# Optimization experiments

Hardware: AMD Instinct MI355X
Metric: run time of the kernel (lower is better)

Reference implementation:

```python
import jax, jax.numpy as jnp
import numpy as np

D_MODEL = 1024
N_HEADS = 16
D_HEAD = D_MODEL // N_HEADS
D_FF = 4096
BATCH = 2
SEQ = 2048
LN_EPS = 1e-5


def setup_inputs() -> dict:
    key = jax.random.key(0)
    ks = jax.random.split(key, 12)
    s = 1.0 / np.sqrt(D_MODEL)
    x = jax.random.normal(ks[0], (BATCH, SEQ, D_MODEL), dtype=jnp.float32)
    mask = jnp.broadcast_to(jnp.tril(jnp.ones((SEQ, SEQ), jnp.int32)), (BATCH, SEQ, SEQ))
    return {
        "x": x,
        "mask": mask,
        # per-head projections stacked: [H, D, Dh] (bias=False in source)
        "Wq": jax.random.normal(ks[1], (N_HEADS, D_MODEL, D_HEAD), jnp.float32) * s,
        "Wk": jax.random.normal(ks[2], (N_HEADS, D_MODEL, D_HEAD), jnp.float32) * s,
        "Wv": jax.random.normal(ks[3], (N_HEADS, D_MODEL, D_HEAD), jnp.float32) * s,
        "Wo": jax.random.normal(ks[4], (D_MODEL, D_MODEL), jnp.float32) * s,
        "ln1_w": jnp.ones((D_MODEL,), jnp.float32),
        "ln1_b": jnp.zeros((D_MODEL,), jnp.float32),
        "ln2_w": jnp.ones((D_MODEL,), jnp.float32),
        "ln2_b": jnp.zeros((D_MODEL,), jnp.float32),
        "W1": jax.random.normal(ks[5], (D_MODEL, D_FF), jnp.float32) * s,
        "b1": jnp.zeros((D_FF,), jnp.float32),
        "W2": jax.random.normal(ks[6], (D_FF, D_MODEL), jnp.float32) * (1.0 / np.sqrt(D_FF)),
        "b2": jnp.zeros((D_MODEL,), jnp.float32),
    }


def layer_norm(x, w, b):
    mu = jnp.mean(x, axis=-1, keepdims=True)
    var = jnp.var(x, axis=-1, keepdims=True)
    return (x - mu) * jax.lax.rsqrt(var + LN_EPS) * w + b


def reference(x, mask, Wq, Wk, Wv, Wo, ln1_w, ln1_b, ln2_w, ln2_b, W1, b1, W2, b2):
    # pre-LN masked self-attention
    h = layer_norm(x, ln1_w, ln1_b)
    q = jnp.einsum("bsd,hde->bhse", h, Wq)  # [B,H,S,Dh]
    k = jnp.einsum("bsd,hde->bhse", h, Wk)
    v = jnp.einsum("bsd,hde->bhse", h, Wv)
    scores = jnp.einsum("bhse,bhte->bhst", q, k) / np.sqrt(D_HEAD)
    scores = jnp.where(mask[:, None, :, :].astype(bool), scores, -jnp.inf)
    weights = jax.nn.softmax(scores, axis=-1)
    attn = jnp.einsum("bhst,bhte->bhse", weights, v)  # [B,H,S,Dh]
    # concat heads (head order = last-dim order in torch.cat)
    concat = attn.transpose(0, 2, 1, 3).reshape(x.shape[0], x.shape[1], D_MODEL)
    att_out = concat @ Wo
    att_x = x + att_out
    # FFN with exact (erf) GELU, matching nn.GELU default
    h2 = layer_norm(att_x, ln2_w, ln2_b)
    ff = jax.nn.gelu(h2 @ W1 + b1, approximate=False) @ W2 + b2
    return att_x + ff
```

## Files before the change

kernel.cpp:

```cpp
#include <hip/hip_runtime.h>
#include <hip/hip_bf16.h>
#include <math.h>

#define D_MODEL 1024
#define N_HEADS 16
#define D_HEAD  64
#define D_FF    4096
#define BATCH   2
#define SEQ     2048
#define NTOK    (BATCH*SEQ)

typedef __hip_bfloat16 bf16;
typedef __attribute__((ext_vector_type(8))) short short8;
typedef __attribute__((ext_vector_type(4))) float floatx4;

template<typename TIN>
__global__ void ln_kernel(const TIN* __restrict__ x,
                          const float* __restrict__ w,
                          const float* __restrict__ b,
                          bf16* __restrict__ out) {
    int row = blockIdx.x;
    int tid = threadIdx.x;
    const long base = (long)row * D_MODEL;
    float v[4];
    float s = 0.f, sq = 0.f;
#pragma unroll
    for (int i = 0; i < 4; ++i) {
        float xv = (float)x[base + tid + i*256];
        v[i] = xv; s += xv; sq += xv*xv;
    }
    __shared__ float r1[256], r2[256];
    r1[tid] = s; r2[tid] = sq; __syncthreads();
    for (int off = 128; off > 0; off >>= 1) {
        if (tid < off) { r1[tid] += r1[tid+off]; r2[tid] += r2[tid+off]; }
        __syncthreads();
    }
    float mean = r1[0] * (1.f/D_MODEL);
    float var  = r2[0] * (1.f/D_MODEL) - mean*mean;
    float rstd = rsqrtf(var + 1e-5f);
#pragma unroll
    for (int i = 0; i < 4; ++i) {
        int c = tid + i*256;
        out[base + c] = __float2bfloat16((v[i] - mean) * rstd * w[c] + b[c]);
    }
}

__global__ __launch_bounds__(256) void wcvt_kernel(const float* __restrict__ W,
                                                   bf16* __restrict__ Wt,
                                                   int K, int N) {
    __shared__ float t[32][33];
    int n0 = blockIdx.x * 32, k0 = blockIdx.y * 32;
    int lx = threadIdx.x & 31, ly = threadIdx.x >> 5;
#pragma unroll
    for (int i = 0; i < 4; ++i) {
        int k = ly + i * 8;
        t[k][lx] = W[(long)(k0 + k) * N + n0 + lx];
    }
    __syncthreads();
#pragma unroll
    for (int i = 0; i < 4; ++i) {
        int n = ly + i * 8;
        Wt[(long)(n0 + n) * K + k0 + lx] = __float2bfloat16(t[lx][n]);
    }
}

__global__ __launch_bounds__(256) void wcvt_wo_w1(const float* __restrict__ Wo,
                                                  const float* __restrict__ W1,
                                                  bf16* __restrict__ wo_bf,
                                                  bf16* __restrict__ w1_bf) {
    __shared__ float t[32][33];
    int gx = blockIdx.x;
    const float* W; bf16* Wt; int N, n0;
    if (gx < 32) { W = Wo; Wt = wo_bf; N = D_MODEL; n0 = gx * 32; }
    else         { W = W1; Wt = w1_bf; N = D_FF;    n0 = (gx - 32) * 32; }
    int k0 = blockIdx.y * 32;
    int lx = threadIdx.x & 31, ly = threadIdx.x >> 5;
#pragma unroll
    for (int i = 0; i < 4; ++i) {
        int k = ly + i * 8;
        t[k][lx] = W[(long)(k0 + k) * N + n0 + lx];
    }
    __syncthreads();
#pragma unroll
    for (int i = 0; i < 4; ++i) {
        int n = ly + i * 8;
        Wt[(long)(n0 + n) * D_MODEL + k0 + lx] = __float2bfloat16(t[lx][n]);
    }
}

__global__ __launch_bounds__(256) void wcvt_qkv(const float* __restrict__ Wq,
                                                const float* __restrict__ Wk,
                                                const float* __restrict__ Wv,
                                                bf16* __restrict__ outp) {
    __shared__ float t[32][33];
    int z = blockIdx.z, mat = z >> 4, head = z & 15;
    const float* W = (mat == 0 ? Wq : mat == 1 ? Wk : Wv) + (long)head * D_MODEL * D_HEAD;
    bf16* Wt = outp + (long)z * D_HEAD * D_MODEL;
    int n0 = blockIdx.x * 32, k0 = blockIdx.y * 32;
    int lx = threadIdx.x & 31, ly = threadIdx.x >> 5;
#pragma unroll
    for (int i = 0; i < 4; ++i) {
        int k = ly + i * 8;
        t[k][lx] = W[(long)(k0 + k) * D_HEAD + n0 + lx];
    }
    __syncthreads();
#pragma unroll
    for (int i = 0; i < 4; ++i) {
        int n = ly + i * 8;
        Wt[(long)(n0 + n) * D_MODEL + k0 + lx] = __float2bfloat16(t[lx][n]);
    }
}

template<int ROWS>
__device__ inline void stage_tile(const bf16* g, int gstride, short* lds) {
    int lane = threadIdx.x & 63, wave = threadIdx.x >> 6;
#pragma unroll
    for (int it = 0; it < ROWS / 64; ++it) {
        int c = wave + it * 4;
        const bf16* gp = g + (long)(c * 16 + (lane >> 2)) * gstride + (lane & 3) * 8;
        short* lp = lds + c * 512 + lane * 8;
        __builtin_amdgcn_global_load_lds(
            (const __attribute__((address_space(1))) void*)gp,
            (__attribute__((address_space(3))) void*)lp, 16, 0, 0);
    }
}

template<int BM, int BN>
__device__ inline void gemm_accum(const bf16* __restrict__ A, int lda,
                                  const bf16* __restrict__ Wt, int K,
                                  int row0, int col0, short* As, short* Bs,
                                  floatx4 (&acc)[BM/32][BN/32]) {
    constexpr int MI = BM / 32;
    constexpr int NR = BN / 32;
    int tid  = threadIdx.x;
    int wave = tid >> 6, lane = tid & 63;
    int quad = lane >> 4, l16 = lane & 15;
    int wm = (wave >> 1) * (BM / 2);
    int wn = (wave & 1) * (BN / 2);

    for (int k0 = 0; k0 < K; k0 += 64) {
        stage_tile<BM>(A  + (long)row0 * lda + k0,      lda, As);
        stage_tile<BM>(A  + (long)row0 * lda + k0 + 32, lda, As + BM * 32);
        stage_tile<BN>(Wt + (long)col0 * K   + k0,      K,   Bs);
        stage_tile<BN>(Wt + (long)col0 * K   + k0 + 32, K,   Bs + BN * 32);
        __syncthreads();

#pragma unroll
        for (int p = 0; p < 2; ++p) {
            const short* Ap = As + p * BM * 32;
            const short* Bp = Bs + p * BN * 32;
            short8 af[MI], bfr[NR];
#pragma unroll
            for (int mi = 0; mi < MI; ++mi)
                af[mi] = *(const short8*)&Ap[(wm + mi * 16 + l16) * 32 + quad * 8];
#pragma unroll
            for (int ni = 0; ni < NR; ++ni)
                bfr[ni] = *(const short8*)&Bp[(wn + ni * 16 + l16) * 32 + quad * 8];
#pragma unroll
            for (int mi = 0; mi < MI; ++mi)
#pragma unroll
                for (int ni = 0; ni < NR; ++ni)
                    acc[mi][ni] = __builtin_amdgcn_mfma_f32_16x16x32_bf16(
                        af[mi], bfr[ni], acc[mi][ni], 0, 0, 0);
        }
        __syncthreads();
    }
}

template<int BM, int BN, int BIAS, int ACT, int RES, int OUTBF16>
__global__ __launch_bounds__(256) void mfma_gemm_bf(
    const bf16* __restrict__ A, int lda,
    const bf16* __restrict__ Wt, int K,
    const float* __restrict__ bias, const float* __restrict__ resid,
    void* __restrict__ Cout, int ldc)
{
    constexpr int MI = BM / 32;
    constexpr int NR = BN / 32;
    __shared__ short As[BM * 64];
    __shared__ short Bs[BN * 64];
    int row0 = blockIdx.y * BM, col0 = blockIdx.x * BN;
    int tid = threadIdx.x, wave = tid >> 6, lane = tid & 63;
    int quad = lane >> 4, l16 = lane & 15;
    int wm = (wave >> 1) * (BM / 2);
    int wn = (wave & 1) * (BN / 2);

    floatx4 acc[MI][NR];
#pragma unroll
    for (int mi = 0; mi < MI; ++mi)
#pragma unroll
        for (int ni = 0; ni < NR; ++ni)
            acc[mi][ni] = (floatx4){0.f, 0.f, 0.f, 0.f};

    gemm_accum<BM, BN>(A, lda, Wt, K, row0, col0, As, Bs, acc);

#pragma unroll
    for (int mi = 0; mi < MI; ++mi) {
#pragma unroll
        for (int ni = 0; ni < NR; ++ni) {
#pragma unroll
            for (int r = 0; r < 4; ++r) {
                int row = row0 + wm + mi * 16 + quad * 4 + r;
                int col = col0 + wn + ni * 16 + l16;
                float v = acc[mi][ni][r];
                if (BIAS) v += bias[col];
                if (ACT == 1) {
                    float x2 = v * v;
                    float arg = fminf(v * fmaf(0.1029392f, x2, 2.3021182f), 20.f);
                    float t = exp2f(arg);
                    v = v * t * __builtin_amdgcn_rcpf(t + 1.f);
                }
                long idx = (long)row * ldc + col;
                if (RES == 1) v += resid[idx];
                if (OUTBF16) ((bf16*)Cout)[idx] = __float2bfloat16(v);
                else         ((float*)Cout)[idx] = v;
            }
        }
    }
}

struct QkvOut { bf16* o[3]; };
__global__ __launch_bounds__(256) void qkv_kernel(const bf16* __restrict__ h1,
                                                  const bf16* __restrict__ wqkv,
                                                  QkvOut a) {
    __shared__ short As[128 * 64];
    __shared__ short Bs[128 * 64];
    int row0 = blockIdx.y * 128, col0 = blockIdx.x * 128;
    int tid = threadIdx.x, wave = tid >> 6, lane = tid & 63;
    int quad = lane >> 4, l16 = lane & 15;
    int wm = (wave >> 1) * 64, wn = (wave & 1) * 64;

    floatx4 acc[4][4];
#pragma unroll
    for (int mi = 0; mi < 4; ++mi)
#pragma unroll
        for (int ni = 0; ni < 4; ++ni)
            acc[mi][ni] = (floatx4){0.f, 0.f, 0.f, 0.f};

    gemm_accum<128, 128>(h1, D_MODEL, wqkv, D_MODEL, row0, col0, As, Bs, acc);

#pragma unroll
    for (int mi = 0; mi < 4; ++mi) {
#pragma unroll
        for (int ni = 0; ni < 4; ++ni) {
#pragma unroll
            for (int r = 0; r < 4; ++r) {
                int row = row0 + wm + mi * 16 + quad * 4 + r;
                int c   = col0 + wn + ni * 16 + l16;
                int mat = c >> 10, hd = (c >> 6) & 15, d = c & 63;
                int b = row >> 11, s = row & 2047;
                a.o[mat][(((long)(b * 16 + hd) * SEQ + s) << 6) + d] =
                    __float2bfloat16(acc[mi][ni][r]);
            }
        }
    }
}

__global__ __launch_bounds__(256) void fattn_mfma(const bf16* __restrict__ q,
                                                  const bf16* __restrict__ k,
                                                  const bf16* __restrict__ v,
                                                  bf16* __restrict__ concat) {
    int byr = blockIdx.y;
    int tile = (byr < 8) ? byr : 23 - byr;
    int bh = blockIdx.x;
    int b  = bh >> 4, h = bh & 15;
    int tid = threadIdx.x;
    int wave = tid >> 6, lane = tid & 63;
    int quad = lane >> 4, l16 = lane & 15;
    const long base = (long)bh * SEQ * D_HEAD;
    const int r0g = tile * 128;

    __shared__ short Ks[64 * 72];
    __shared__ short Vt[64 * 72];
    __shared__ short Ps[4][32 * 72];

    short8 qf[2][2];
#pragma unroll
    for (int rb = 0; rb < 2; ++rb) {
        const short* qrow = (const short*)(q + base +
            (long)(r0g + wave * 32 + rb * 16 + l16) * D_HEAD);
        qf[rb][0] = *(const short8*)(qrow + quad * 8);
        qf[rb][1] = *(const short8*)(qrow + 32 + quad * 8);
#pragma unroll
        for (int c = 0; c < 2; ++c)
#pragma unroll
            for (int j = 0; j < 8; ++j) {
                float f = __uint_as_float(((unsigned)(unsigned short)qf[rb][c][j]) << 16)
                          * 0.18033688f;
                qf[rb][c][j] = __builtin_bit_cast(short, __float2bfloat16(f));
            }
    }

    short8 onesf;
    {
        short o1 = (l16 == 0) ? (short)0x3F80 : (short)0;
#pragma unroll
        for (int j = 0; j < 8; ++j) onesf[j] = o1;
    }

    floatx4 o[2][4];
#pragma unroll
    for (int rb = 0; rb < 2; ++rb)
#pragma unroll
        for (int nb = 0; nb < 4; ++nb) o[rb][nb] = (floatx4){0.f, 0.f, 0.f, 0.f};
    floatx4 l4[2] = {(floatx4){0.f,0.f,0.f,0.f}, (floatx4){0.f,0.f,0.f,0.f}};

    const int ktmax = 2 * tile + 1;
    for (int kt = 0; kt <= ktmax; ++kt) {
        __syncthreads();
        {
            int t = tid >> 2, c = tid & 3;
            const short* krow = (const short*)(k + base + (long)(kt * 64 + t) * D_HEAD);
            *(uint4*)&Ks[t * 72 + c * 16]     = *(const uint4*)(krow + c * 16);
            *(uint4*)&Ks[t * 72 + c * 16 + 8] = *(const uint4*)(krow + c * 16 + 8);
        }
        {
            int tp = (tid & 31) * 2;
            int d0 = ((tid >> 5) & 7) * 8;
            const short* v0 = (const short*)(v + base + (long)(kt * 64 + tp) * D_HEAD + d0);
            short va[8], vb[8];
            *(uint4*)va = *(const uint4*)v0;
            *(uint4*)vb = *(const uint4*)(v0 + D_HEAD);
#pragma unroll
            for (int j = 0; j < 8; ++j) {
                unsigned pk = (unsigned)(unsigned short)va[j] |
                              ((unsigned)(unsigned short)vb[j] << 16);
                *(unsigned*)&Vt[(d0 + j) * 72 + tp] = pk;
            }
        }
        __syncthreads();

        if (kt * 64 > r0g + wave * 32 + 31) continue;

        floatx4 s[2][4];
#pragma unroll
        for (int nb = 0; nb < 4; ++nb) {
            short8 kf0 = *(const short8*)&Ks[(nb * 16 + l16) * 72 + quad * 8];
            short8 kf1 = *(const short8*)&Ks[(nb * 16 + l16) * 72 + 32 + quad * 8];
#pragma unroll
            for (int rb = 0; rb < 2; ++rb) {
                floatx4 z4 = (floatx4){0.f, 0.f, 0.f, 0.f};
                z4 = __builtin_amdgcn_mfma_f32_16x16x32_bf16(qf[rb][0], kf0, z4, 0, 0, 0);
                z4 = __builtin_amdgcn_mfma_f32_16x16x32_bf16(qf[rb][1], kf1, z4, 0, 0, 0);
                s[rb][nb] = z4;
            }
        }

        if (kt >= 2 * tile) {
#pragma unroll
            for (int rb = 0; rb < 2; ++rb) {
                int qg = r0g + wave * 32 + rb * 16 + quad * 4;
#pragma unroll
                for (int nb = 0; nb < 4; ++nb) {
                    int kg = kt * 64 + nb * 16 + l16;
#pragma unroll
                    for (int r = 0; r < 4; ++r)
                        if (kg > qg + r) s[rb][nb][r] = -1e30f;
                }
            }
        }

        short* Pw = &Ps[wave][0];
#pragma unroll
        for (int rb = 0; rb < 2; ++rb)
#pragma unroll
            for (int nb = 0; nb < 4; ++nb)
#pragma unroll
                for (int r = 0; r < 4; ++r) {
                    float p = exp2f(s[rb][nb][r]);
                    Pw[(rb * 16 + quad * 4 + r) * 72 + nb * 16 + l16] =
                        __builtin_bit_cast(short, __float2bfloat16(p));
                }

        short8 pf[2][2];
#pragma unroll
        for (int rb = 0; rb < 2; ++rb) {
            pf[rb][0] = *(const short8*)&Pw[(rb * 16 + l16) * 72 + quad * 8];
            pf[rb][1] = *(const short8*)&Pw[(rb * 16 + l16) * 72 + 32 + quad * 8];
        }
#pragma unroll
        for (int nb = 0; nb < 4; ++nb) {
            short8 vf0 = *(const short8*)&Vt[(nb * 16 + l16) * 72 + quad * 8];
            short8 vf1 = *(const short8*)&Vt[(nb * 16 + l16) * 72 + 32 + quad * 8];
#pragma unroll
            for (int rb = 0; rb < 2; ++rb) {
                o[rb][nb] = __builtin_amdgcn_mfma_f32_16x16x32_bf16(pf[rb][0], vf0, o[rb][nb], 0, 0, 0);
                o[rb][nb] = __builtin_amdgcn_mfma_f32_16x16x32_bf16(pf[rb][1], vf1, o[rb][nb], 0, 0, 0);
            }
        }
#pragma unroll
        for (int rb = 0; rb < 2; ++rb) {
            l4[rb] = __builtin_amdgcn_mfma_f32_16x16x32_bf16(pf[rb][0], onesf, l4[rb], 0, 0, 0);
            l4[rb] = __builtin_amdgcn_mfma_f32_16x16x32_bf16(pf[rb][1], onesf, l4[rb], 0, 0, 0);
        }
    }

#pragma unroll
    for (int rb = 0; rb < 2; ++rb) {
        float linv[4];
#pragma unroll
        for (int r = 0; r < 4; ++r) {
            float lv = __shfl(l4[rb][r], lane & 48);
            linv[r] = 1.f / lv;
        }
#pragma unroll
        for (int nb = 0; nb < 4; ++nb)
#pragma unroll
            for (int r = 0; r < 4; ++r) {
                int row = r0g + wave * 32 + rb * 16 + quad * 4 + r;
                int col = h * D_HEAD + nb * 16 + l16;
                concat[(long)(b * SEQ + row) * D_MODEL + col] =
                    __float2bfloat16(o[rb][nb][r] * linv[r]);
            }
    }
}

extern "C" void kernel_launch(void* const* d_in, const int* in_sizes, int n_in,
                              void* d_out, int out_size, void* d_ws, size_t ws_size,
                              hipStream_t stream) {
    const float* x    = (const float*)d_in[0];
    const float* Wq   = (const float*)d_in[2];
    const float* Wk   = (const float*)d_in[3];
    const float* Wv   = (const float*)d_in[4];
    const float* Wo   = (const float*)d_in[5];
    const float* ln1w = (const float*)d_in[6];
    const float* ln1b = (const float*)d_in[7];
    const float* ln2w = (const float*)d_in[8];
    const float* ln2b = (const float*)d_in[9];
    const float* W1   = (const float*)d_in[10];
    const float* b1   = (const float*)d_in[11];
    const float* W2   = (const float*)d_in[12];
    const float* b2   = (const float*)d_in[13];
    float* out = (float*)d_out;

    char* wsb = (char*)d_ws;
    const size_t MB = 1024*1024;
    bf16*  h1      = (bf16*)(wsb + 0*MB);
    bf16*  qb      = (bf16*)(wsb + 8*MB);
    bf16*  kb      = (bf16*)(wsb + 16*MB);
    bf16*  vb      = (bf16*)(wsb + 24*MB);
    bf16*  wqkv_bf = (bf16*)(wsb + 32*MB);
    bf16*  cc      = (bf16*)(wsb + 0*MB);
    bf16*  wo_bf   = (bf16*)(wsb + 8*MB);
    bf16*  w1_bf   = (bf16*)(wsb + 10*MB);
    bf16*  h2      = (bf16*)(wsb + 0*MB);
    bf16*  ff      = (bf16*)(wsb + 24*MB);
    bf16*  w2_bf   = (bf16*)(wsb + 8*MB);

    ln_kernel<float><<<NTOK, 256, 0, stream>>>(x, ln1w, ln1b, h1);

    wcvt_qkv<<<dim3(2, 32, 48), 256, 0, stream>>>(Wq, Wk, Wv, wqkv_bf);

    QkvOut qa; qa.o[0] = qb; qa.o[1] = kb; qa.o[2] = vb;
    qkv_kernel<<<dim3(24, 32), 256, 0, stream>>>(h1, wqkv_bf, qa);

    fattn_mfma<<<dim3(BATCH*N_HEADS, SEQ/128), 256, 0, stream>>>(qb, kb, vb, cc);

    wcvt_wo_w1<<<dim3(160, 32), 256, 0, stream>>>(Wo, W1, wo_bf, w1_bf);

    mfma_gemm_bf<64,128,0,0,1,0><<<dim3(8,64), 256, 0, stream>>>(
        cc, D_MODEL, wo_bf, D_MODEL, nullptr, x, out, D_MODEL);

    ln_kernel<float><<<NTOK, 256, 0, stream>>>(out, ln2w, ln2b, h2);

    mfma_gemm_bf<128,128,1,1,0,1><<<dim3(32,32), 256, 0, stream>>>(
        h2, D_MODEL, w1_bf, D_MODEL, b1, nullptr, ff, D_FF);

    wcvt_kernel<<<dim3(D_MODEL/32, D_FF/32), 256, 0, stream>>>(W2, w2_bf, D_FF, D_MODEL);

    mfma_gemm_bf<64,128,1,0,1,0><<<dim3(8,64), 256, 0, stream>>>(
        ff, D_FF, w2_bf, D_FF, b2, out, out, D_MODEL);
}
```

Before: 384.8 us.

## Split causal attention KV range into two chunks with separate combine kernel

The flash attention kernel now launches a third grid dimension that splits each query tile's key range in two, so every block handles about half the keys. It writes unnormalized partial outputs in bf16 plus per-row denominators, and a new combine kernel sums the two partials and normalizes into the concat buffer. This doubles the block count to fill more compute units during attention. The cost is an extra kernel launch, an extra round trip through memory for the partial outputs, and an added bf16 rounding of the partials. It relies on the softmax using a fixed scale with no running max, so partials can be added directly.

```diff
diff --git a/kernel.cpp b/kernel.cpp
--- a/kernel.cpp
+++ b/kernel.cpp
@@ -258,17 +258,21 @@
 __global__ __launch_bounds__(256) void fattn_mfma(const bf16* __restrict__ q,
                                                   const bf16* __restrict__ k,
                                                   const bf16* __restrict__ v,
-                                                  bf16* __restrict__ concat) {
+                                                  bf16* __restrict__ po,
+                                                  float* __restrict__ lz) {
     int byr = blockIdx.y;
     int tile = (byr < 8) ? byr : 23 - byr;
+    int chunk = blockIdx.z;
     int bh = blockIdx.x;
-    int b  = bh >> 4, h = bh & 15;
     int tid = threadIdx.x;
     int wave = tid >> 6, lane = tid & 63;
     int quad = lane >> 4, l16 = lane & 15;
     const long base = (long)bh * SEQ * D_HEAD;
     const int r0g = tile * 128;
 
+    bf16*  pob = po + (long)chunk * 32 * SEQ * 64;
+    float* lzb = lz + (long)chunk * 32 * SEQ;
+
     __shared__ short Ks[64 * 72];
     __shared__ short Vt[64 * 72];
     __shared__ short Ps[4][32 * 72];
@@ -304,8 +308,9 @@
         for (int nb = 0; nb < 4; ++nb) o[rb][nb] = (floatx4){0.f, 0.f, 0.f, 0.f};
     floatx4 l4[2] = {(floatx4){0.f,0.f,0.f,0.f}, (floatx4){0.f,0.f,0.f,0.f}};
 
-    const int ktmax = 2 * tile + 1;
-    for (int kt = 0; kt <= ktmax; ++kt) {
+    const int kt0 = chunk ? tile + 1 : 0;
+    const int kt1 = chunk ? 2 * tile + 1 : tile;
+    for (int kt = kt0; kt <= kt1; ++kt) {
         __syncthreads();
         {
             int t = tid >> 2, c = tid & 3;
@@ -396,22 +401,50 @@
 
 #pragma unroll
     for (int rb = 0; rb < 2; ++rb) {
-        float linv[4];
-#pragma unroll
-        for (int r = 0; r < 4; ++r) {
-            float lv = __shfl(l4[rb][r], lane & 48);
-            linv[r] = 1.f / lv;
-        }
 #pragma unroll
         for (int nb = 0; nb < 4; ++nb)
 #pragma unroll
             for (int r = 0; r < 4; ++r) {
                 int row = r0g + wave * 32 + rb * 16 + quad * 4 + r;
-                int col = h * D_HEAD + nb * 16 + l16;
-                concat[(long)(b * SEQ + row) * D_MODEL + col] =
-                    __float2bfloat16(o[rb][nb][r] * linv[r]);
-            }
-    }
+                pob[((long)bh * SEQ + row) * 64 + nb * 16 + l16] =
+                    __float2bfloat16(o[rb][nb][r]);
+            }
+        if (l16 == 0) {
+#pragma unroll
+            for (int r = 0; r < 4; ++r) {
+                int row = r0g + wave * 32 + rb * 16 + quad * 4 + r;
+                lzb[(long)bh * SEQ + row] = l4[rb][r];
+            }
+        }
+    }
+}
+
+__global__ __launch_bounds__(256) void attn_combine(const bf16* __restrict__ po,
+                                                    const float* __restrict__ lz,
+                                                    bf16* __restrict__ cc) {
+    const long CH = 32L * SEQ * 64;
+    int row = blockIdx.x;
+    int b = row >> 11, s = row & 2047;
+    int tid = threadIdx.x;
+    int col = tid * 4;
+    int h = col >> 6, d = col & 63;
+    long pidx = ((long)(b * 16 + h) * SEQ + s) * 64 + d;
+    uint2 u0 = *(const uint2*)((const unsigned short*)po + pidx);
+    uint2 u1 = *(const uint2*)((const unsigned short*)po + CH + pidx);
+    long li = (long)(b * 16 + h) * SEQ + s;
+    float linv = 1.f / (lz[li] + lz[32L * SEQ + li]);
+    unsigned ua[4] = {u0.x & 0xFFFFu, u0.x >> 16, u0.y & 0xFFFFu, u0.y >> 16};
+    unsigned ub[4] = {u1.x & 0xFFFFu, u1.x >> 16, u1.y & 0xFFFFu, u1.y >> 16};
+    unsigned short rr[4];
+#pragma unroll
+    for (int i = 0; i < 4; ++i) {
+        float ov = __uint_as_float(ua[i] << 16) + __uint_as_float(ub[i] << 16);
+        rr[i] = __builtin_bit_cast(unsigned short, __float2bfloat16(ov * linv));
+    }
+    uint2 w;
+    w.x = (unsigned)rr[0] | ((unsigned)rr[1] << 16);
+    w.y = (unsigned)rr[2] | ((unsigned)rr[3] << 16);
+    *(uint2*)((unsigned short*)cc + (long)row * D_MODEL + col) = w;
 }
 
 extern "C" void kernel_launch(void* const* d_in, const int* in_sizes, int n_in,
@@ -439,6 +472,8 @@
     bf16*  kb      = (bf16*)(wsb + 16*MB);
     bf16*  vb      = (bf16*)(wsb + 24*MB);
     bf16*  wqkv_bf = (bf16*)(wsb + 32*MB);
+    bf16*  po      = (bf16*)(wsb + 32*MB);
+    float* lz      = (float*)(wsb + 48*MB);
     bf16*  cc      = (bf16*)(wsb + 0*MB);
     bf16*  wo_bf   = (bf16*)(wsb + 8*MB);
     bf16*  w1_bf   = (bf16*)(wsb + 10*MB);
@@ -453,7 +488,9 @@
     QkvOut qa; qa.o[0] = qb; qa.o[1] = kb; qa.o[2] = vb;
     qkv_kernel<<<dim3(24, 32), 256, 0, stream>>>(h1, wqkv_bf, qa);
 
-    fattn_mfma<<<dim3(BATCH*N_HEADS, SEQ/128), 256, 0, stream>>>(qb, kb, vb, cc);
+    fattn_mfma<<<dim3(BATCH*N_HEADS, SEQ/128, 2), 256, 0, stream>>>(qb, kb, vb, po, lz);
+
+    attn_combine<<<NTOK, 256, 0, stream>>>(po, lz, cc);
 
     wcvt_wo_w1<<<dim3(160, 32), 256, 0, stream>>>(Wo, W1, wo_bf, w1_bf);
 
```

Result: no change. 379.2 us (-1.5%).
